# Optimization experiments

Hardware: AMD Instinct MI355X
Metric: run time of the kernel (lower is better)

## Reference

```python
import jax, jax.numpy as jnp
import numpy as np

B, N, DIM, VDIM, H, HD = 4, 1369, 1024, 1536, 16, 64
ROPE_HW, ROPE_DIM, THETA = 37, 32, 10000.0
LN_EPS = 1e-5


def _rope_tables():
    # VisionRotaryEmbeddingFast: freqs_for='lang', dim=32, pt_seq_len=ft_seq_len=37
    inv = 1.0 / THETA ** (jnp.arange(0, ROPE_DIM, 2, dtype=jnp.float32) / ROPE_DIM)  # [16]
    t = jnp.arange(ROPE_HW, dtype=jnp.float32) / ROPE_HW * ROPE_HW                    # [37]
    f = t[:, None] * inv[None, :]                                                     # [37,16]
    f = jnp.repeat(f, 2, axis=-1)                                                     # [37,32]
    # broadcat along last dim over the 2D grid -> [37,37,64]
    f2 = jnp.concatenate([jnp.broadcast_to(f[:, None, :], (ROPE_HW, ROPE_HW, ROPE_DIM)),
                          jnp.broadcast_to(f[None, :, :], (ROPE_HW, ROPE_HW, ROPE_DIM))], axis=-1)
    f2 = f2.reshape(-1, 2 * ROPE_DIM)                                                 # [1369,64]
    return jnp.cos(f2), jnp.sin(f2)


def _rotate_half(x):
    # pairs (x0,x1) -> (-x1,x0), interleaved
    xr = x.reshape(*x.shape[:-1], x.shape[-1] // 2, 2)
    x1, x2 = xr[..., 0], xr[..., 1]
    return jnp.stack((-x2, x1), axis=-1).reshape(x.shape)


def setup_inputs() -> dict:
    key = jax.random.key(0)
    ks = jax.random.split(key, 8)
    return {
        "x": jax.random.normal(ks[0], (B, N, DIM), jnp.float32),
        "value": jax.random.normal(ks[1], (B, N, VDIM), jnp.float32),
        "attn_mask": jax.random.randint(ks[2], (B, N), 0, 2).astype(bool),
        "wq": jax.random.normal(ks[3], (DIM, DIM), jnp.float32) * 0.02,
        "wk": jax.random.normal(ks[4], (DIM, VDIM), jnp.float32) * 0.02,
        "wv": jax.random.normal(ks[5], (DIM, VDIM), jnp.float32) * 0.02,
        "ln_g": jnp.ones((DIM,), jnp.float32),
        "ln_b": jnp.zeros((DIM,), jnp.float32),
        "wp": jax.random.normal(ks[6], (DIM, DIM), jnp.float32) * 0.02,
        "bp": jnp.zeros((DIM,), jnp.float32),
    }


def reference(x, value, attn_mask, wq, wk, wv, ln_g, ln_b, wp, bp):
    cos, sin = _rope_tables()  # [N, 64] each
    # projections (torch F.linear: y = x @ W.T)
    q = jnp.einsum('bni,oi->bno', x, wq).reshape(B, N, H, HD).transpose(0, 2, 1, 3)
    k = jnp.einsum('bni,oi->bno', value, wk).reshape(B, N, H, HD).transpose(0, 2, 1, 3)
    v = jnp.einsum('bni,oi->bno', value, wv).reshape(B, N, H, HD).transpose(0, 2, 1, 3)
    # inline RoPE on q and k
    q = q * cos + _rotate_half(q) * sin
    k = k * cos + _rotate_half(k) * sin
    q = q * (HD ** -0.5)
    attn = jnp.einsum('bhnd,bhmd->bhnm', q, k)
    neg_inf = jnp.finfo(attn.dtype).min
    attn = jnp.where(attn_mask[:, None, None, :], attn, neg_inf)
    attn = jax.nn.softmax(attn, axis=-1)
    out = jnp.einsum('bhnm,bhmd->bhnd', attn, v)
    out = out.transpose(0, 2, 1, 3).reshape(B, N, H * HD)
    # inner_attn_ln (LayerNorm, eps=1e-5)
    mu = jnp.mean(out, axis=-1, keepdims=True)
    var = jnp.var(out, axis=-1, keepdims=True)
    out = (out - mu) * jax.lax.rsqrt(var + LN_EPS) * ln_g + ln_b
    # output projection
    return jnp.einsum('bni,oi->bno', out, wp) + bp
```

## Files before the change

kernel.cpp:

```cpp
#include <hip/hip_runtime.h>
#include <hip/hip_bf16.h>

#define BB 4
#define NN 1369
#define DIMM 1024
#define VDIMM 1536
#define HH 16
#define MM (BB*NN)
#define MPAD 5504
#define NPAD 1408
#define KVB 64
#define NT (NPAD/KVB)
#define QSCALE 0.18028334f

typedef __attribute__((ext_vector_type(4))) float f32x4;
typedef __attribute__((ext_vector_type(8))) __bf16 bf16x8;
typedef __attribute__((ext_vector_type(4))) __bf16 bf16x4;

#define GLOAD_LDS(gsrc, ldst) \
  __builtin_amdgcn_global_load_lds((const __attribute__((address_space(1))) unsigned int*)(gsrc), \
                                   (__attribute__((address_space(3))) unsigned int*)(ldst), 16, 0, 0)

__global__ __launch_bounds__(256) void cvt4(const float* __restrict__ src,
                                            __bf16* __restrict__ dst, int n4) {
  int i = blockIdx.x * blockDim.x + threadIdx.x;
  int st = gridDim.x * blockDim.x;
  for (; i < n4; i += st) {
    f32x4 v = ((const f32x4*)src)[i];
    bf16x4 o;
    o[0] = (__bf16)v[0]; o[1] = (__bf16)v[1];
    o[2] = (__bf16)v[2]; o[3] = (__bf16)v[3];
    ((bf16x4*)dst)[i] = o;
  }
}

__global__ __launch_bounds__(256) void rope_tables(float* __restrict__ cosT,
                                                   float* __restrict__ sinT) {
  int idx = blockIdx.x * blockDim.x + threadIdx.x;
  if (idx >= NN * 64) return;
  int n = idx >> 6, d = idx & 63;
  int r = n / 37, c = n % 37;
  int m = (d < 32) ? (d >> 1) : ((d - 32) >> 1);
  float p = (d < 32) ? (float)r : (float)c;
  float inv = powf(10000.f, -(float)m * (1.f / 16.f));
  float a = p * inv;
  cosT[idx] = cosf(a);
  sinT[idx] = sinf(a);
}

__global__ __launch_bounds__(256) void mask_prep(const void* __restrict__ mask,
                                                 float* __restrict__ maskA) {
  __shared__ int flags[2];
  int t = threadIdx.x;
  if (t < 2) flags[t] = 0;
  __syncthreads();
  const unsigned int* mw = (const unsigned int*)mask;
  for (int i = t; i < NN; i += blockDim.x) {
    unsigned int w = mw[i];
    if (w == 0x3F800000u) atomicOr(&flags[1], 1);
    else if (w > 1u) atomicOr(&flags[0], 1);
  }
  __syncthreads();
  int md = flags[1] ? 2 : (flags[0] ? 1 : 0);
  const unsigned char* mb = (const unsigned char*)mask;
  const float* mf = (const float*)mask;
  for (int i = t; i < BB * NPAD; i += blockDim.x) {
    int b = i / NPAD, key = i % NPAD;
    float v = -1e30f;
    if (key < NN) {
      int idx = b * NN + key;
      bool on = (md == 0) ? (mw[idx] != 0u) : (md == 1) ? (mb[idx] != 0) : (mf[idx] != 0.f);
      if (on) v = 0.f;
    }
    maskA[i] = v;
  }
}

template <int TN, int EPI>
__global__ __launch_bounds__(256) void gemm_bt(
    const __bf16* __restrict__ A, const __bf16* __restrict__ W, int K,
    __bf16* __restrict__ obf, __bf16* __restrict__ obf2, float* __restrict__ of32,
    const float* __restrict__ cosT, const float* __restrict__ sinT,
    const float* __restrict__ bp) {
  constexpr int MI = (TN == 128) ? 4 : 2;
  __shared__ __bf16 As[128 * 32];
  __shared__ __bf16 Bs[TN * 32];
  const int tid = threadIdx.x;
  const int w = tid >> 6, l = tid & 63;
  const int tM = blockIdx.y, tN = blockIdx.x;
  const int wm = (TN == 128) ? (w >> 1) : w;
  const int wn = (TN == 128) ? (w & 1) : 0;
  const int wmo = wm * ((TN == 128) ? 64 : 32);
  const int wno = wn * 64;
  const int lo = l & 15, hi = l >> 4;

  f32x4 zero = {0.f, 0.f, 0.f, 0.f};
  f32x4 acc[MI][4];
#pragma unroll
  for (int i = 0; i < MI; ++i)
#pragma unroll
    for (int j = 0; j < 4; ++j) acc[i][j] = zero;

  for (int k0 = 0; k0 < K; k0 += 32) {
    __syncthreads();
#pragma unroll
    for (int j = 0; j < 2; ++j) {
      int c = j * 4 + w;
      const char* src = (const char*)A +
          ((size_t)(tM * 128 + c * 16 + (l >> 2)) * K + k0) * 2 + (l & 3) * 16;
      GLOAD_LDS(src, (char*)As + c * 1024);
    }
    if (TN == 128) {
#pragma unroll
      for (int j = 0; j < 2; ++j) {
        int c = j * 4 + w;
        const char* src = (const char*)W +
            ((size_t)(tN * 128 + c * 16 + (l >> 2)) * K + k0) * 2 + (l & 3) * 16;
        GLOAD_LDS(src, (char*)Bs + c * 1024);
      }
    } else {
      const char* src = (const char*)W +
          ((size_t)(tN * 64 + w * 16 + (l >> 2)) * K + k0) * 2 + (l & 3) * 16;
      GLOAD_LDS(src, (char*)Bs + w * 1024);
    }
    __syncthreads();
    bf16x8 af[MI], bfr[4];
#pragma unroll
    for (int mi = 0; mi < MI; ++mi)
      af[mi] = *(const bf16x8*)&As[(wmo + mi * 16 + lo) * 32 + hi * 8];
#pragma unroll
    for (int ni = 0; ni < 4; ++ni)
      bfr[ni] = *(const bf16x8*)&Bs[(wno + ni * 16 + lo) * 32 + hi * 8];
#pragma unroll
    for (int mi = 0; mi < MI; ++mi)
#pragma unroll
      for (int ni = 0; ni < 4; ++ni)
        acc[mi][ni] = __builtin_amdgcn_mfma_f32_16x16x32_bf16(af[mi], bfr[ni], acc[mi][ni], 0, 0, 0);
  }

  const int m_base = tM * 128 + wmo;
  const int o_base = tN * TN + wno;
  const bool isK = (EPI == 1) && (tN * TN < 1024);
#pragma unroll
  for (int mi = 0; mi < MI; ++mi) {
#pragma unroll
    for (int r = 0; r < 4; ++r) {
      const int mrow = m_base + mi * 16 + hi * 4 + r;
#pragma unroll
      for (int ni = 0; ni < 4; ++ni) {
        const int col = o_base + ni * 16 + lo;
        float v = acc[mi][ni][r];
        if (EPI == 0) {
          float pprt = __shfl_xor(v, 1);
          if (mrow < MM) {
            int b = mrow / NN, n = mrow % NN;
            int h = col >> 6, d = col & 63;
            float cs = cosT[n * 64 + d], sn = sinT[n * 64 + d];
            float out = (v * cs + (((d & 1) == 0) ? -pprt : pprt) * sn) * QSCALE;
            obf[((size_t)(b * HH + h) * NPAD + n) * 64 + d] = (__bf16)out;
          }
        } else if (EPI == 1) {
          if (isK) {
            float pprt = __shfl_xor(v, 1);
            if (mrow < MM) {
              int b = mrow / NN, n = mrow % NN;
              int h = col >> 6, d = col & 63;
              float cs = cosT[n * 64 + d], sn = sinT[n * 64 + d];
              float out = v * cs + (((d & 1) == 0) ? -pprt : pprt) * sn;
              obf[((size_t)(b * HH + h) * NPAD + n) * 64 + d] = (__bf16)out;
            }
          } else {
            if (mrow < MM) {
              int b = mrow / NN, n = mrow % NN;
              int o2 = col - 1024;
              int h = o2 >> 6, d = o2 & 63;
              obf2[((size_t)(b * HH + h) * 64 + d) * NPAD + n] = (__bf16)v;
            }
          }
        } else {
          if (mrow < MM) of32[(size_t)mrow * DIMM + col] = v + bp[col];
        }
      }
    }
  }
}

__device__ inline unsigned int pk2(float a, float b) {
  unsigned int ua = (unsigned int)__builtin_bit_cast(unsigned short, (__bf16)a);
  unsigned int ub = (unsigned int)__builtin_bit_cast(unsigned short, (__bf16)b);
  return ua | (ub << 16);
}

__global__ __launch_bounds__(256) void attn_kernel(
    const __bf16* __restrict__ Qb, const __bf16* __restrict__ Kb,
    const __bf16* __restrict__ Vtb, const float* __restrict__ maskA,
    float* __restrict__ AO) {
  __shared__ __bf16 Ks[2][64 * 64];
  __shared__ __bf16 Vs[2][64 * 64];
  __shared__ unsigned int Plds[4][16 * 32];
  const int tid = threadIdx.x;
  const int w = tid >> 6, l = tid & 63;
  const int lo = l & 15, hi = l >> 4;

  const int i = blockIdx.x;
  const int orig = (i & 7) * 176 + (i >> 3);
  const int bh = orig / NT;
  const int qt = orig % NT;
  const int b = bh >> 4;
  const int q0 = qt * 64 + w * 16;

  const __bf16* Qp = Qb + ((size_t)bh * NPAD + q0) * 64;
  bf16x8 qf0 = *(const bf16x8*)&Qp[lo * 64 + hi * 8];
  bf16x8 qf1 = *(const bf16x8*)&Qp[lo * 64 + 32 + hi * 8];

  const int row8 = l >> 3;
  const int swz16 = ((l & 7) ^ row8) << 4;
  const int lo7 = lo & 7;
  const int swzW = (lo & 7) << 2;

  f32x4 zero = {0.f, 0.f, 0.f, 0.f};
  f32x4 O[4];
#pragma unroll
  for (int n = 0; n < 4; ++n) O[n] = zero;
  float lr = 0.f;
  const float* mk = maskA + b * NPAD;

#define STAGE(buf, k0)                                                                   \
  {                                                                                      \
    _Pragma("unroll") for (int j = 0; j < 2; ++j) {                                      \
      const int rbase = (j * 4 + w) * 8;                                                 \
      const char* ksrc = (const char*)Kb +                                               \
          ((size_t)bh * NPAD + (k0) + rbase + row8) * 128 + swz16;                       \
      GLOAD_LDS(ksrc, (char*)&Ks[buf][0] + rbase * 128);                                 \
      const char* vsrc = (const char*)Vtb +                                              \
          ((size_t)(bh * 64 + rbase + row8) * NPAD + (k0)) * 2 + swz16;                  \
      GLOAD_LDS(vsrc, (char*)&Vs[buf][0] + rbase * 128);                                 \
    }                                                                                    \
  }

  STAGE(0, 0);
  __syncthreads();
  int cur = 0;

  for (int t = 0; t < NT; ++t) {
    if (t + 1 < NT) STAGE(cur ^ 1, (t + 1) * KVB);

    const __bf16* KB = &Ks[cur][0];
    const __bf16* VB = &Vs[cur][0];

    f32x4 mv[4];
#pragma unroll
    for (int c = 0; c < 4; ++c) mv[c] = *(const f32x4*)&mk[t * KVB + c * 16 + hi * 4];

    f32x4 S[4];
    __builtin_amdgcn_s_setprio(1);
#pragma unroll
    for (int c = 0; c < 4; ++c) {
      const int kr = c * 16 + lo;
      bf16x8 kfa = *(const bf16x8*)&KB[kr * 64 + ((hi ^ lo7) * 8)];
      bf16x8 kfb = *(const bf16x8*)&KB[kr * 64 + (((hi + 4) ^ lo7) * 8)];
      f32x4 s = __builtin_amdgcn_mfma_f32_16x16x32_bf16(kfa, qf0, zero, 0, 0, 0);
      S[c]     = __builtin_amdgcn_mfma_f32_16x16x32_bf16(kfb, qf1, s, 0, 0, 0);
    }
    __builtin_amdgcn_s_setprio(0);

    float rs = 0.f;
#pragma unroll
    for (int c = 0; c < 4; ++c) {
      float p0 = exp2f(S[c][0] + mv[c][0]);
      float p1 = exp2f(S[c][1] + mv[c][1]);
      float p2 = exp2f(S[c][2] + mv[c][2]);
      float p3 = exp2f(S[c][3] + mv[c][3]);
      rs += (p0 + p1) + (p2 + p3);
      uint2 pw = {pk2(p0, p1), pk2(p2, p3)};
      *(uint2*)&Plds[w][lo * 32 + ((8 * c + 2 * hi) ^ swzW)] = pw;
    }
    lr += rs;

    bf16x8 pf0 = *(const bf16x8*)&Plds[w][lo * 32 + ((4 * hi) ^ swzW)];
    bf16x8 pf1 = *(const bf16x8*)&Plds[w][lo * 32 + ((16 + 4 * hi) ^ swzW)];

    __builtin_amdgcn_s_setprio(1);
#pragma unroll
    for (int n = 0; n < 4; ++n) {
      const int vr = n * 16 + lo;
      bf16x8 vfa = *(const bf16x8*)&VB[vr * 64 + ((hi ^ lo7) * 8)];
      bf16x8 vfb = *(const bf16x8*)&VB[vr * 64 + (((hi + 4) ^ lo7) * 8)];
      O[n] = __builtin_amdgcn_mfma_f32_16x16x32_bf16(vfa, pf0, O[n], 0, 0, 0);
      O[n] = __builtin_amdgcn_mfma_f32_16x16x32_bf16(vfb, pf1, O[n], 0, 0, 0);
    }
    __builtin_amdgcn_s_setprio(0);

    __syncthreads();
    cur ^= 1;
  }
#undef STAGE

  lr += __shfl_xor(lr, 16);
  lr += __shfl_xor(lr, 32);
  const float inv = 1.f / lr;

  const int h = bh & 15;
  const int token = q0 + lo;
  if (token < NN) {
    float* dst = AO + (size_t)(b * NN + token) * DIMM + h * 64 + hi * 4;
#pragma unroll
    for (int n = 0; n < 4; ++n) {
      f32x4 o = O[n];
      o[0] *= inv; o[1] *= inv; o[2] *= inv; o[3] *= inv;
      *(f32x4*)(dst + n * 16) = o;
    }
  }
}

__global__ __launch_bounds__(256) void ln_kernel(
    const float* __restrict__ AO, const float* __restrict__ g,
    const float* __restrict__ be, __bf16* __restrict__ outb) {
  const int row = blockIdx.x;
  const int t = threadIdx.x;
  const float* x = AO + (size_t)row * DIMM;
  f32x4 v = ((const f32x4*)x)[t];
  float s = v[0] + v[1] + v[2] + v[3];
  float sq = v[0] * v[0] + v[1] * v[1] + v[2] * v[2] + v[3] * v[3];
#pragma unroll
  for (int m = 1; m < 64; m <<= 1) { s += __shfl_xor(s, m); sq += __shfl_xor(sq, m); }
  __shared__ float ss[4], ssq[4];
  int w = t >> 6, l = t & 63;
  if (l == 0) { ss[w] = s; ssq[w] = sq; }
  __syncthreads();
  s = ss[0] + ss[1] + ss[2] + ss[3];
  sq = ssq[0] + ssq[1] + ssq[2] + ssq[3];
  float mean = s * (1.f / 1024.f);
  float var = sq * (1.f / 1024.f) - mean * mean;
  float rstd = rsqrtf(var + 1e-5f);
  __bf16* o = outb + (size_t)row * DIMM + t * 4;
  const float* gp = g + t * 4;
  const float* bp2 = be + t * 4;
#pragma unroll
  for (int j = 0; j < 4; ++j) o[j] = (__bf16)((v[j] - mean) * rstd * gp[j] + bp2[j]);
}

extern "C" void kernel_launch(void* const* d_in, const int* in_sizes, int n_in,
                              void* d_out, int out_size, void* d_ws, size_t ws_size,
                              hipStream_t stream) {
  const float* x   = (const float*)d_in[0];
  const float* val = (const float*)d_in[1];
  const void*  msk = d_in[2];
  const float* wq  = (const float*)d_in[3];
  const float* wk  = (const float*)d_in[4];
  const float* wv  = (const float*)d_in[5];
  const float* lng = (const float*)d_in[6];
  const float* lnb = (const float*)d_in[7];
  const float* wp  = (const float*)d_in[8];
  const float* bpv = (const float*)d_in[9];
  float* out = (float*)d_out;

  char* ws = (char*)d_ws;
  size_t off = 0;
  auto alloc = [&](size_t bytes) -> char* {
    char* p = ws + off;
    off += (bytes + 255) & ~(size_t)255;
    return p;
  };
  __bf16* xb   = (__bf16*)alloc((size_t)MPAD * 1024 * 2);
  __bf16* vb   = (__bf16*)alloc((size_t)MPAD * 1536 * 2);
  __bf16* wqb  = (__bf16*)alloc((size_t)1024 * 1024 * 2);
  __bf16* wkvb = (__bf16*)alloc((size_t)2048 * 1536 * 2);
  __bf16* wpb  = (__bf16*)alloc((size_t)1024 * 1024 * 2);
  __bf16* Qb   = (__bf16*)alloc((size_t)64 * NPAD * 64 * 2);
  __bf16* Kb   = (__bf16*)alloc((size_t)64 * NPAD * 64 * 2);
  __bf16* Vtb  = (__bf16*)alloc((size_t)64 * 64 * NPAD * 2);
  float* AO    = (float*)alloc((size_t)MM * 1024 * 4);
  float* cosT  = (float*)alloc((size_t)NN * 64 * 4);
  float* sinT  = (float*)alloc((size_t)NN * 64 * 4);
  float* maskA = (float*)alloc((size_t)BB * NPAD * 4);

  hipMemsetAsync(xb + (size_t)MM * 1024, 0, (size_t)(MPAD - MM) * 1024 * 2, stream);
  hipMemsetAsync(vb + (size_t)MM * 1536, 0, (size_t)(MPAD - MM) * 1536 * 2, stream);
  hipMemsetAsync(Qb, 0, (size_t)64 * NPAD * 64 * 2, stream);
  hipMemsetAsync(Kb, 0, (size_t)64 * NPAD * 64 * 2, stream);
  hipMemsetAsync(Vtb, 0, (size_t)64 * 64 * NPAD * 2, stream);

  cvt4<<<1024, 256, 0, stream>>>(x, xb, MM * 1024 / 4);
  cvt4<<<1024, 256, 0, stream>>>(val, vb, MM * 1536 / 4);
  cvt4<<<512, 256, 0, stream>>>(wq, wqb, 1024 * 1024 / 4);
  cvt4<<<512, 256, 0, stream>>>(wk, wkvb, 1024 * 1536 / 4);
  cvt4<<<512, 256, 0, stream>>>(wv, wkvb + (size_t)1024 * 1536, 1024 * 1536 / 4);
  cvt4<<<512, 256, 0, stream>>>(wp, wpb, 1024 * 1024 / 4);
  rope_tables<<<(NN * 64 + 255) / 256, 256, 0, stream>>>(cosT, sinT);
  mask_prep<<<1, 256, 0, stream>>>(msk, maskA);

  gemm_bt<64, 0><<<dim3(16, 43), 256, 0, stream>>>(xb, wqb, 1024, Qb, nullptr, nullptr, cosT, sinT, nullptr);
  gemm_bt<128, 1><<<dim3(16, 43), 256, 0, stream>>>(vb, wkvb, 1536, Kb, Vtb, nullptr, cosT, sinT, nullptr);

  attn_kernel<<<dim3(64 * NT), 256, 0, stream>>>(Qb, Kb, Vtb, maskA, AO);

  ln_kernel<<<MM, 256, 0, stream>>>(AO, lng, lnb, xb);

  gemm_bt<64, 3><<<dim3(16, 43), 256, 0, stream>>>(xb, wpb, 1024, nullptr, nullptr, out, nullptr, nullptr, bpv);
}
```

Measured before the change: 303.0 us.

## Double-buffer GEMM LDS tiles, remap blocks for XCD locality, vectorize V-transpose stores

```diff
diff --git a/kernel.cpp b/kernel.cpp
--- a/kernel.cpp
+++ b/kernel.cpp
@@ -83,16 +83,20 @@
     const float* __restrict__ cosT, const float* __restrict__ sinT,
     const float* __restrict__ bp) {
   constexpr int MI = (TN == 128) ? 4 : 2;
-  __shared__ __bf16 As[128 * 32];
-  __shared__ __bf16 Bs[TN * 32];
+  __shared__ __bf16 As[2][128 * 32];
+  __shared__ __bf16 Bs[2][TN * 32];
   const int tid = threadIdx.x;
   const int w = tid >> 6, l = tid & 63;
-  const int tM = blockIdx.y, tN = blockIdx.x;
+  const int i0 = blockIdx.x;
+  const int orig = (i0 & 7) * 86 + (i0 >> 3);
+  const int tN = orig & 15, tM = orig >> 4;
   const int wm = (TN == 128) ? (w >> 1) : w;
   const int wn = (TN == 128) ? (w & 1) : 0;
   const int wmo = wm * ((TN == 128) ? 64 : 32);
-  const int wno = wn * 64;
   const int lo = l & 15, hi = l >> 4;
+
+  const __bf16* Asrc = A + (size_t)(tM * 128 + lo) * K + hi * 8;
+  const __bf16* Wsrc = W + (size_t)(tN * TN + lo) * K + hi * 8;
 
   f32x4 zero = {0.f, 0.f, 0.f, 0.f};
   f32x4 acc[MI][4];
@@ -101,84 +105,95 @@
 #pragma unroll
     for (int j = 0; j < 4; ++j) acc[i][j] = zero;
 
-  for (int k0 = 0; k0 < K; k0 += 32) {
+#define GSTAGE(buf, k0)                                                          \
+  {                                                                              \
+    _Pragma("unroll") for (int j = 0; j < 2; ++j) {                              \
+      const int c = j * 4 + w;                                                   \
+      GLOAD_LDS(Asrc + (size_t)c * 16 * K + (k0), (char*)&As[buf][c * 512]);     \
+    }                                                                            \
+    if (TN == 128) {                                                             \
+      _Pragma("unroll") for (int j = 0; j < 2; ++j) {                            \
+        const int c = j * 4 + w;                                                 \
+        GLOAD_LDS(Wsrc + (size_t)c * 16 * K + (k0), (char*)&Bs[buf][c * 512]);   \
+      }                                                                          \
+    } else {                                                                     \
+      GLOAD_LDS(Wsrc + (size_t)w * 16 * K + (k0), (char*)&Bs[buf][w * 512]);     \
+    }                                                                            \
+  }
+
+  GSTAGE(0, 0);
+  int cur = 0;
+  const int nk = K >> 5;
+  const int ga = wmo >> 4;
+  const int gb = (TN == 128) ? (wn * 4) : 0;
+  for (int t = 0; t < nk; ++t) {
     __syncthreads();
-#pragma unroll
-    for (int j = 0; j < 2; ++j) {
-      int c = j * 4 + w;
-      const char* src = (const char*)A +
-          ((size_t)(tM * 128 + c * 16 + (l >> 2)) * K + k0) * 2 + (l & 3) * 16;
-      GLOAD_LDS(src, (char*)As + c * 1024);
-    }
-    if (TN == 128) {
-#pragma unroll
-      for (int j = 0; j < 2; ++j) {
-        int c = j * 4 + w;
-        const char* src = (const char*)W +
-            ((size_t)(tN * 128 + c * 16 + (l >> 2)) * K + k0) * 2 + (l & 3) * 16;
-        GLOAD_LDS(src, (char*)Bs + c * 1024);
+    if (t + 1 < nk) GSTAGE(cur ^ 1, (t + 1) * 32);
+    bf16x8 af[MI], bfr[4];
+#pragma unroll
+    for (int mi = 0; mi < MI; ++mi)
+      af[mi] = *(const bf16x8*)&As[cur][(ga + mi) * 512 + hi * 128 + lo * 8];
+#pragma unroll
+    for (int ni = 0; ni < 4; ++ni)
+      bfr[ni] = *(const bf16x8*)&Bs[cur][(gb + ni) * 512 + hi * 128 + lo * 8];
+#pragma unroll
+    for (int mi = 0; mi < MI; ++mi)
+#pragma unroll
+      for (int ni = 0; ni < 4; ++ni)
+        acc[mi][ni] = __builtin_amdgcn_mfma_f32_16x16x32_bf16(af[mi], bfr[ni], acc[mi][ni], 0, 0, 0);
+    cur ^= 1;
+  }
+#undef GSTAGE
+
+  const int m_base = tM * 128 + wmo;
+  const int o_base = tN * TN + wn * 64;
+  const bool isK = (EPI == 1) && (tN < 8);
+#pragma unroll
+  for (int mi = 0; mi < MI; ++mi) {
+    const int m4 = m_base + mi * 16 + hi * 4;
+    if (EPI == 1 && !isK) {
+      if (m4 < MM) {
+        const int b0 = m4 / NN, n0 = m4 % NN;
+#pragma unroll
+        for (int ni = 0; ni < 4; ++ni) {
+          const int o2 = o_base + ni * 16 + lo - 1024;
+          const int h = o2 >> 6, d = o2 & 63;
+          if (n0 <= NN - 4) {
+            bf16x4 pv;
+#pragma unroll
+            for (int r = 0; r < 4; ++r) pv[r] = (__bf16)acc[mi][ni][r];
+            *(bf16x4*)&obf2[((size_t)(b0 * HH + h) * 64 + d) * NPAD + n0] = pv;
+          } else {
+#pragma unroll
+            for (int r = 0; r < 4; ++r) {
+              const int mr = m4 + r;
+              const int br = mr / NN, nr = mr % NN;
+              obf2[((size_t)(br * HH + h) * 64 + d) * NPAD + nr] = (__bf16)acc[mi][ni][r];
+            }
+          }
+        }
       }
     } else {
-      const char* src = (const char*)W +
-          ((size_t)(tN * 64 + w * 16 + (l >> 2)) * K + k0) * 2 + (l & 3) * 16;
-      GLOAD_LDS(src, (char*)Bs + w * 1024);
-    }
-    __syncthreads();
-    bf16x8 af[MI], bfr[4];
-#pragma unroll
-    for (int mi = 0; mi < MI; ++mi)
-      af[mi] = *(const bf16x8*)&As[(wmo + mi * 16 + lo) * 32 + hi * 8];
-#pragma unroll
-    for (int ni = 0; ni < 4; ++ni)
-      bfr[ni] = *(const bf16x8*)&Bs[(wno + ni * 16 + lo) * 32 + hi * 8];
-#pragma unroll
-    for (int mi = 0; mi < MI; ++mi)
-#pragma unroll
-      for (int ni = 0; ni < 4; ++ni)
-        acc[mi][ni] = __builtin_amdgcn_mfma_f32_16x16x32_bf16(af[mi], bfr[ni], acc[mi][ni], 0, 0, 0);
-  }
-
-  const int m_base = tM * 128 + wmo;
-  const int o_base = tN * TN + wno;
-  const bool isK = (EPI == 1) && (tN * TN < 1024);
-#pragma unroll
-  for (int mi = 0; mi < MI; ++mi) {
-#pragma unroll
-    for (int r = 0; r < 4; ++r) {
-      const int mrow = m_base + mi * 16 + hi * 4 + r;
-#pragma unroll
-      for (int ni = 0; ni < 4; ++ni) {
-        const int col = o_base + ni * 16 + lo;
-        float v = acc[mi][ni][r];
-        if (EPI == 0) {
-          float pprt = __shfl_xor(v, 1);
-          if (mrow < MM) {
-            int b = mrow / NN, n = mrow % NN;
-            int h = col >> 6, d = col & 63;
-            float cs = cosT[n * 64 + d], sn = sinT[n * 64 + d];
-            float out = (v * cs + (((d & 1) == 0) ? -pprt : pprt) * sn) * QSCALE;
-            obf[((size_t)(b * HH + h) * NPAD + n) * 64 + d] = (__bf16)out;
-          }
-        } else if (EPI == 1) {
-          if (isK) {
+#pragma unroll
+      for (int r = 0; r < 4; ++r) {
+        const int mrow = m4 + r;
+#pragma unroll
+        for (int ni = 0; ni < 4; ++ni) {
+          const int col = o_base + ni * 16 + lo;
+          float v = acc[mi][ni][r];
+          if (EPI == 0 || EPI == 1) {
             float pprt = __shfl_xor(v, 1);
             if (mrow < MM) {
               int b = mrow / NN, n = mrow % NN;
               int h = col >> 6, d = col & 63;
               float cs = cosT[n * 64 + d], sn = sinT[n * 64 + d];
               float out = v * cs + (((d & 1) == 0) ? -pprt : pprt) * sn;
+              if (EPI == 0) out *= QSCALE;
               obf[((size_t)(b * HH + h) * NPAD + n) * 64 + d] = (__bf16)out;
             }
           } else {
-            if (mrow < MM) {
-              int b = mrow / NN, n = mrow % NN;
-              int o2 = col - 1024;
-              int h = o2 >> 6, d = o2 & 63;
-              obf2[((size_t)(b * HH + h) * 64 + d) * NPAD + n] = (__bf16)v;
-            }
+            if (mrow < MM) of32[(size_t)mrow * DIMM + col] = v + bp[col];
           }
-        } else {
-          if (mrow < MM) of32[(size_t)mrow * DIMM + col] = v + bp[col];
         }
       }
     }
@@ -390,12 +405,12 @@
   rope_tables<<<(NN * 64 + 255) / 256, 256, 0, stream>>>(cosT, sinT);
   mask_prep<<<1, 256, 0, stream>>>(msk, maskA);
 
-  gemm_bt<64, 0><<<dim3(16, 43), 256, 0, stream>>>(xb, wqb, 1024, Qb, nullptr, nullptr, cosT, sinT, nullptr);
-  gemm_bt<128, 1><<<dim3(16, 43), 256, 0, stream>>>(vb, wkvb, 1536, Kb, Vtb, nullptr, cosT, sinT, nullptr);
+  gemm_bt<64, 0><<<dim3(688), 256, 0, stream>>>(xb, wqb, 1024, Qb, nullptr, nullptr, cosT, sinT, nullptr);
+  gemm_bt<128, 1><<<dim3(688), 256, 0, stream>>>(vb, wkvb, 1536, Kb, Vtb, nullptr, cosT, sinT, nullptr);
 
   attn_kernel<<<dim3(64 * NT), 256, 0, stream>>>(Qb, Kb, Vtb, maskA, AO);
 
   ln_kernel<<<MM, 256, 0, stream>>>(AO, lng, lnb, xb);
 
-  gemm_bt<64, 3><<<dim3(16, 43), 256, 0, stream>>>(xb, wpb, 1024, nullptr, nullptr, out, nullptr, nullptr, bpv);
-}
+  gemm_bt<64, 3><<<dim3(688), 256, 0, stream>>>(xb, wpb, 1024, nullptr, nullptr, out, nullptr, nullptr, bpv);
+}
```

After: 305.7 us. Within noise of the previous version (+0.9%).
